# Kernel tuning notes

Hardware: AMD Instinct MI355X
Metric: run time of the kernel (lower is better)

## Reference

```python
import jax, jax.numpy as jnp
import numpy as np

R = 7        # rcnn_crop_size[cls_ind]
SCALE = 4    # cfg['stride']


def _pool1d(x, c0, c1, K):
    # Adaptive max pool along leading axis of x ([F, ...] -> [R, ...]).
    # torch AdaptiveMaxPool bins: start_i = floor(i*L/R), end_i = ceil((i+1)*L/R)
    F = x.shape[0]
    L = c1 - c0
    i = jnp.arange(R)
    starts = c0 + (i * L) // R
    ends = c0 + ((i + 1) * L + R - 1) // R
    idx = starts[:, None] + jnp.arange(K)[None, :]           # [R, K], K bounds max bin length
    g = x[jnp.clip(idx, 0, F - 1)]                           # [R, K, ...]
    valid = (idx < ends[:, None]).reshape((R, K) + (1,) * (x.ndim - 1))
    return jnp.max(jnp.where(valid, g, jnp.finfo(x.dtype).min), axis=1)


def _crop_pool(f, dims_max, p, Ks):
    # One proposal: variable-size crop from f[b] + adaptive max pool to [C,R,R,R].
    b = p[0].astype(jnp.int32)
    center, side = p[2:5], p[5:8]
    c0 = jnp.floor((center - side / 2) / SCALE).astype(jnp.int32)
    c1 = jnp.ceil((center + side / 2) / SCALE).astype(jnp.int32)
    c0 = jnp.maximum(c0, 0)
    c1 = jnp.minimum(c1, dims_max)
    x = f[b]                                                 # [C, Fd, Fh, Fw]
    for ax in range(3):                                      # separable adaptive max pool
        x = jnp.moveaxis(x, ax + 1, 0)
        x = _pool1d(x, c0[ax], c1[ax], Ks[ax])
        x = jnp.moveaxis(x, 0, ax + 1)
    return x                                                 # [C, R, R, R]


def setup_inputs() -> dict:
    key = jax.random.key(0)
    kf, kb, ks, kc, kd = jax.random.split(key, 5)
    B, C, Fs = 4, 64, 32
    N = 96
    f = jax.random.normal(kf, (B, C, Fs, Fs, Fs), dtype=jnp.float32)
    inputs = jnp.zeros((B, 1, 128, 128, 128), dtype=jnp.float32)
    bidx = jax.random.randint(kb, (N, 1), 0, B).astype(jnp.float32)
    score = jax.random.uniform(ks, (N, 1), dtype=jnp.float32)
    centers = jax.random.uniform(kc, (N, 3), minval=24.0, maxval=104.0, dtype=jnp.float32)
    sides = jax.random.uniform(kd, (N, 3), minval=8.0, maxval=48.0, dtype=jnp.float32)
    proposals = jnp.concatenate([bidx, score, centers, sides], axis=1)  # [N, 8]
    return {"f": f, "inputs": inputs, "proposals": proposals, "cls_ind": 0}


def reference(f, inputs, proposals, cls_ind):
    D, H, W = inputs.shape[2], inputs.shape[3], inputs.shape[4]
    dims_max = jnp.array([D // SCALE, H // SCALE, W // SCALE], dtype=jnp.int32)
    # max bin length per axis for any crop length L <= F: ceil(F/R)+1
    Ks = tuple(-(-f.shape[ax + 2] // R) + 1 for ax in range(3))
    return jax.vmap(lambda p: _crop_pool(f, dims_max, p, Ks))(proposals)  # [N, C, R, R, R]
```

## Files before the change

### kernel.cpp

```cpp
#include <hip/hip_runtime.h>
#include <float.h>


__global__ void crop_roi_kernel(const float* __restrict__ f,
                                const float* __restrict__ props,
                                float* __restrict__ out,
                                int C, int total) {
    const int F = 32;
    const int DIMS = 32;
    int t = blockIdx.x * blockDim.x + threadIdx.x;
    if (t >= total) return;

    int k = t % 7;
    int j = (t / 7) % 7;
    int i = (t / 49) % 7;
    int c = (t / 343) % C;
    int n = t / (343 * C);

    const float* p = props + (size_t)n * 8;
    int b = (int)p[0];

    int c0[3], c1[3];
#pragma unroll
    for (int ax = 0; ax < 3; ++ax) {
        float ce = p[2 + ax];
        float sd = p[5 + ax];
        int lo = (int)floorf((ce - sd * 0.5f) * 0.25f);
        int hi = (int)ceilf((ce + sd * 0.5f) * 0.25f);
        lo = lo > 0 ? lo : 0;
        hi = hi < DIMS ? hi : DIMS;
        c0[ax] = lo;
        c1[ax] = hi;
    }
    int L0 = c1[0] - c0[0];
    int L1 = c1[1] - c0[1];
    int L2 = c1[2] - c0[2];

    int ds = c0[0] + (i * L0) / 7;
    int de = c0[0] + ((i + 1) * L0 + 6) / 7;
    int hs = c0[1] + (j * L1) / 7;
    int he = c0[1] + ((j + 1) * L1 + 6) / 7;
    int ws = c0[2] + (k * L2) / 7;
    int we = c0[2] + ((k + 1) * L2 + 6) / 7;

    float m = -FLT_MAX;
    const float* base = f + ((size_t)b * C + c) * (F * F * F);
    for (int d = ds; d < de; ++d) {
        for (int h = hs; h < he; ++h) {
            const float* row = base + (d * F + h) * F;
            for (int w = ws; w < we; ++w) {
                m = fmaxf(m, row[w]);
            }
        }
    }
    out[t] = m;
}

extern "C" void kernel_launch(void* const* d_in, const int* in_sizes, int n_in,
                              void* d_out, int out_size, void* d_ws, size_t ws_size,
                              hipStream_t stream) {
    const float* f = (const float*)d_in[0];
    const float* props = (const float*)d_in[2];

    int N = in_sizes[2] / 8;
    int C = out_size / (N * 343);
    int total = out_size;

    int threads = 256;
    int blocks = (total + threads - 1) / threads;
    crop_roi_kernel<<<blocks, threads, 0, stream>>>(f, props, (float*)d_out, C, total);
}
```

Baseline: 117.7 us.

## Use 3D blocks per proposal-channel and fixed 3x3x3 unrolled bin max

Each block of 7x7x7 threads now handles one (channel, proposal) pair, which removes the per-thread integer div/mod index decoding. Crop lengths up to 14 give bins of at most 3 elements per axis, so those cases use a fully unrolled 27-load max with clamped indices, where duplicate reads do not change the result. Larger crops fall back to the generic loop. The 343-thread blocks leave part of the last wavefront idle, and the per-proposal bounds are recomputed by every thread.

```diff
diff --git a/kernel.cpp b/kernel.cpp
--- a/kernel.cpp
+++ b/kernel.cpp
@@ -2,58 +2,71 @@
 #include <float.h>
 
 
-__global__ void crop_roi_kernel(const float* __restrict__ f,
-                                const float* __restrict__ props,
-                                float* __restrict__ out,
-                                int C, int total) {
-    const int F = 32;
+__global__ __launch_bounds__(343) void crop_roi_kernel(
+        const float* __restrict__ f,
+        const float* __restrict__ props,
+        float* __restrict__ out,
+        int C) {
     const int DIMS = 32;
-    int t = blockIdx.x * blockDim.x + threadIdx.x;
-    if (t >= total) return;
-
-    int k = t % 7;
-    int j = (t / 7) % 7;
-    int i = (t / 49) % 7;
-    int c = (t / 343) % C;
-    int n = t / (343 * C);
+    const int c = blockIdx.x;
+    const int n = blockIdx.y;
+    const int k = threadIdx.x;
+    const int j = threadIdx.y;
+    const int i = threadIdx.z;
 
     const float* p = props + (size_t)n * 8;
-    int b = (int)p[0];
+    const int b = (int)p[0];
 
-    int c0[3], c1[3];
+    int d0 = (int)floorf((p[2] - p[5] * 0.5f) * 0.25f);
+    int d1 = (int)ceilf((p[2] + p[5] * 0.5f) * 0.25f);
+    int h0 = (int)floorf((p[3] - p[6] * 0.5f) * 0.25f);
+    int h1 = (int)ceilf((p[3] + p[6] * 0.5f) * 0.25f);
+    int w0 = (int)floorf((p[4] - p[7] * 0.5f) * 0.25f);
+    int w1 = (int)ceilf((p[4] + p[7] * 0.5f) * 0.25f);
+    d0 = max(d0, 0); d1 = min(d1, DIMS);
+    h0 = max(h0, 0); h1 = min(h1, DIMS);
+    w0 = max(w0, 0); w1 = min(w1, DIMS);
+    const int Ld = d1 - d0, Lh = h1 - h0, Lw = w1 - w0;
+
+    const int ds = d0 + (i * Ld) / 7,  de = d0 + ((i + 1) * Ld + 6) / 7;
+    const int hs = h0 + (j * Lh) / 7,  he = h0 + ((j + 1) * Lh + 6) / 7;
+    const int ws = w0 + (k * Lw) / 7,  we = w0 + ((k + 1) * Lw + 6) / 7;
+
+    const float* base = f + (((size_t)b * C + c) << 15);
+    float m = -FLT_MAX;
+
+    const bool fast = (Ld >= 1 && Ld <= 14 &&
+                       Lh >= 1 && Lh <= 14 &&
+                       Lw >= 1 && Lw <= 14);
+    if (fast) {
+        const int dA = ds, dB = min(ds + 1, de - 1), dC2 = min(ds + 2, de - 1);
+        const int hA = hs, hB = min(hs + 1, he - 1), hC2 = min(hs + 2, he - 1);
+        const int wA = ws, wB = min(ws + 1, we - 1), wC2 = min(ws + 2, we - 1);
+        const int dd[3] = {dA << 10, dB << 10, dC2 << 10};
+        const int hh[3] = {hA << 5,  hB << 5,  hC2 << 5};
+        const int ww[3] = {wA, wB, wC2};
 #pragma unroll
-    for (int ax = 0; ax < 3; ++ax) {
-        float ce = p[2 + ax];
-        float sd = p[5 + ax];
-        int lo = (int)floorf((ce - sd * 0.5f) * 0.25f);
-        int hi = (int)ceilf((ce + sd * 0.5f) * 0.25f);
-        lo = lo > 0 ? lo : 0;
-        hi = hi < DIMS ? hi : DIMS;
-        c0[ax] = lo;
-        c1[ax] = hi;
-    }
-    int L0 = c1[0] - c0[0];
-    int L1 = c1[1] - c0[1];
-    int L2 = c1[2] - c0[2];
-
-    int ds = c0[0] + (i * L0) / 7;
-    int de = c0[0] + ((i + 1) * L0 + 6) / 7;
-    int hs = c0[1] + (j * L1) / 7;
-    int he = c0[1] + ((j + 1) * L1 + 6) / 7;
-    int ws = c0[2] + (k * L2) / 7;
-    int we = c0[2] + ((k + 1) * L2 + 6) / 7;
-
-    float m = -FLT_MAX;
-    const float* base = f + ((size_t)b * C + c) * (F * F * F);
-    for (int d = ds; d < de; ++d) {
-        for (int h = hs; h < he; ++h) {
-            const float* row = base + (d * F + h) * F;
-            for (int w = ws; w < we; ++w) {
-                m = fmaxf(m, row[w]);
+        for (int x = 0; x < 3; ++x) {
+            const float* pd = base + dd[x];
+#pragma unroll
+            for (int y = 0; y < 3; ++y) {
+                const float* ph = pd + hh[y];
+#pragma unroll
+                for (int z = 0; z < 3; ++z) {
+                    m = fmaxf(m, ph[ww[z]]);
+                }
+            }
+        }
+    } else {
+        for (int d = ds; d < de; ++d) {
+            for (int h = hs; h < he; ++h) {
+                const float* row = base + (d << 10) + (h << 5);
+                for (int w = ws; w < we; ++w) m = fmaxf(m, row[w]);
             }
         }
     }
-    out[t] = m;
+
+    out[((size_t)n * C + c) * 343 + (i * 49 + j * 7 + k)] = m;
 }
 
 extern "C" void kernel_launch(void* const* d_in, const int* in_sizes, int n_in,
@@ -64,9 +77,8 @@
 
     int N = in_sizes[2] / 8;
     int C = out_size / (N * 343);
-    int total = out_size;
 
-    int threads = 256;
-    int blocks = (total + threads - 1) / threads;
-    crop_roi_kernel<<<blocks, threads, 0, stream>>>(f, props, (float*)d_out, C, total);
+    dim3 block(7, 7, 7);
+    dim3 grid(C, N);
+    crop_roi_kernel<<<grid, block, 0, stream>>>(f, props, (float*)d_out, C);
 }
```

Result: slower. 134.9 us (+14.6%).
